# Performance work log

Hardware: AMD Instinct MI355X
Metric: run time of the kernel (lower is better)

Reference implementation:

```python
import jax, jax.numpy as jnp
import numpy as np

B, T, N, D = 64, 10, 64, 4      # batch, time steps, num_vars, input_size
H = 128                          # encoder_hidden
K = 2                            # num_edge_types
EPS = 1e-5                       # BatchNorm eps
_edges = np.ones((N, N)) - np.eye(N)
SEND = jnp.asarray(np.where(_edges)[0])   # [E], E = N*(N-1)
RECV = jnp.asarray(np.where(_edges)[1])   # [E]


def _xavier(key, shape):
    std = (2.0 / (shape[0] + shape[1])) ** 0.5
    return std * jax.random.normal(key, shape, dtype=jnp.float32)


def _mlp(x, w1, b1, w2, b2, g, beta):
    # RefNRIMLP: Linear -> ELU -> (dropout p=0) -> Linear -> ELU -> BatchNorm1d
    h = jax.nn.elu(x @ w1 + b1)
    h = jax.nn.elu(h @ w2 + b2)
    flat = h.reshape(-1, h.shape[-1])  # BN over flattened (batch*objects) axis
    mu = flat.mean(0)
    var = flat.var(0)
    flat = (flat - mu) * jax.lax.rsqrt(var + EPS) * g + beta
    return flat.reshape(h.shape)


def setup_inputs() -> dict:
    key = jax.random.key(0)
    ks = jax.random.split(key, 10)
    inp = {"inputs": jax.random.normal(ks[0], (B, T, N, D), dtype=jnp.float32)}
    fan_ins = {"mlp1": T * D, "mlp2": 2 * H, "mlp3": H, "mlp4": 3 * H}
    for i, (name, nin) in enumerate(fan_ins.items()):
        k1, k2 = jax.random.split(ks[i + 1])
        inp[name + "_w1"] = _xavier(k1, (nin, H))
        inp[name + "_b1"] = jnp.full((H,), 0.1, dtype=jnp.float32)
        inp[name + "_w2"] = _xavier(k2, (H, H))
        inp[name + "_b2"] = jnp.full((H,), 0.1, dtype=jnp.float32)
        inp[name + "_g"] = jnp.ones((H,), dtype=jnp.float32)
        inp[name + "_beta"] = jnp.zeros((H,), dtype=jnp.float32)
    inp["fc_w"] = _xavier(ks[9], (H, K))
    inp["fc_b"] = jnp.full((K,), 0.1, dtype=jnp.float32)
    return inp


def reference(inputs, mlp1_w1, mlp1_b1, mlp1_w2, mlp1_b2, mlp1_g, mlp1_beta,
              mlp2_w1, mlp2_b1, mlp2_w2, mlp2_b2, mlp2_g, mlp2_beta,
              mlp3_w1, mlp3_b1, mlp3_w2, mlp3_b2, mlp3_g, mlp3_beta,
              mlp4_w1, mlp4_b1, mlp4_w2, mlp4_b2, mlp4_g, mlp4_beta,
              fc_w, fc_b):
    # [B,T,N,D] -> [B,N,T*D]
    x = jnp.transpose(inputs, (0, 2, 1, 3)).reshape(B, N, T * D)
    x = _mlp(x, mlp1_w1, mlp1_b1, mlp1_w2, mlp1_b2, mlp1_g, mlp1_beta)
    # node2edge: gather send/recv node embeddings, concat -> [B,E,2H]
    x = jnp.concatenate([x[:, SEND], x[:, RECV]], axis=-1)
    x = _mlp(x, mlp2_w1, mlp2_b1, mlp2_w2, mlp2_b2, mlp2_g, mlp2_beta)
    x_skip = x
    # edge2node: one-hot(recv).T matmul == segment_sum over recv index, then /(N-1)
    agg = jax.ops.segment_sum(jnp.swapaxes(x, 0, 1), RECV, num_segments=N)  # [N,B,H]
    x = jnp.swapaxes(agg, 0, 1) / (N - 1)  # [B,N,H]
    x = _mlp(x, mlp3_w1, mlp3_b1, mlp3_w2, mlp3_b2, mlp3_g, mlp3_beta)
    x = jnp.concatenate([x[:, SEND], x[:, RECV]], axis=-1)  # [B,E,2H]
    x = jnp.concatenate([x, x_skip], axis=-1)  # [B,E,3H]
    x = _mlp(x, mlp4_w1, mlp4_b1, mlp4_w2, mlp4_b2, mlp4_g, mlp4_beta)
    return x @ fc_w + fc_b  # logits [B, E, K]
```

## Files before the change

kernel.cpp:

```cpp
#include <hip/hip_runtime.h>

#define BN_EPS 1e-5f

using h8 = __attribute__((ext_vector_type(8))) _Float16;
using h4v = __attribute__((ext_vector_type(4))) _Float16;
using f4v = __attribute__((ext_vector_type(4))) float;

#define OFF_COEF 0
#define OFF_CVEC 1024
#define OFF_H1 4096
#define OFF_P2 528384
#define OFF_Q2 1052672
#define OFF_H3 1576960
#define OFF_P4 2101248
#define OFF_Q4 2625536
#define OFF_W2P 3149824
#define OFF_W4P 3158016
#define OFF_WCP 3166208
#define OFF_H4B 3174400
#define WS_BYTES 78757888ull

__device__ __forceinline__ float elu_f(float x) {
    return x > 0.f ? x : __expf(x) - 1.f;
}


__device__ __forceinline__ void gemm32_globalW(const float* As, int lda,
                                               const float* __restrict__ Wg, int K,
                                               float acc[2][8], int tx, int ty) {
    const float4* Wg4 = (const float4*)Wg;
#pragma unroll 4
    for (int k = 0; k < K; ++k) {
        float a0 = As[ty * lda + k];
        float a1 = As[(ty + 16) * lda + k];
        float4 wa = Wg4[k * 32 + tx];
        float4 wb = Wg4[k * 32 + 16 + tx];
        const float wv[8] = {wa.x, wa.y, wa.z, wa.w, wb.x, wb.y, wb.z, wb.w};
#pragma unroll
        for (int u = 0; u < 8; ++u) {
            acc[0][u] = fmaf(a0, wv[u], acc[0][u]);
            acc[1][u] = fmaf(a1, wv[u], acc[1][u]);
        }
    }
}

__device__ __forceinline__ void bias_elu32(const float acc[2][8],
                                           const float* __restrict__ bias,
                                           float vals[2][8], int tx) {
    int ca = 4 * tx, cb = 64 + 4 * tx;
    float bv[8] = {bias[ca], bias[ca + 1], bias[ca + 2], bias[ca + 3],
                   bias[cb], bias[cb + 1], bias[cb + 2], bias[cb + 3]};
#pragma unroll
    for (int j = 0; j < 2; ++j)
#pragma unroll
        for (int u = 0; u < 8; ++u)
            vals[j][u] = elu_f(acc[j][u] + bv[u]);
}

__device__ __forceinline__ void store_tile32(float* __restrict__ out, int row0,
                                             const float vals[2][8], int tx, int ty) {
#pragma unroll
    for (int j = 0; j < 2; ++j) {
        int r = row0 + ty + 16 * j;
        *(float4*)(out + r * 128 + 4 * tx) =
            make_float4(vals[j][0], vals[j][1], vals[j][2], vals[j][3]);
        *(float4*)(out + r * 128 + 64 + 4 * tx) =
            make_float4(vals[j][4], vals[j][5], vals[j][6], vals[j][7]);
    }
}

__device__ __forceinline__ void stats_tail32(const float vals[2][8], float* red,
                                             float* __restrict__ st, int tid, int tx, int ty) {
    float ls[8], lq[8];
#pragma unroll
    for (int u = 0; u < 8; ++u) {
        ls[u] = vals[0][u] + vals[1][u];
        lq[u] = vals[0][u] * vals[0][u] + vals[1][u] * vals[1][u];
    }
    __syncthreads();
    int ca = 4 * tx, cb = 64 + 4 * tx;
#pragma unroll
    for (int u = 0; u < 4; ++u) {
        red[ty * 128 + ca + u] = ls[u];
        red[2048 + ty * 128 + ca + u] = lq[u];
        red[ty * 128 + cb + u] = ls[u + 4];
        red[2048 + ty * 128 + cb + u] = lq[u + 4];
    }
    __syncthreads();
    if (tid < 128) {
        float s = 0.f, q = 0.f;
#pragma unroll
        for (int t = 0; t < 16; ++t) {
            s += red[t * 128 + tid];
            q += red[2048 + t * 128 + tid];
        }
        atomicAdd(st + tid, s);
        atomicAdd(st + 128 + tid, q);
    }
}


__device__ __forceinline__ void gemm2_gw(const _Float16* A0, const _Float16* A1,
                                         const _Float16* __restrict__ wp,
                                         f4v acc0[4][2], f4v acc1[4][2], int lane, int w) {
#pragma unroll
    for (int kc = 0; kc < 4; ++kc) {
        h8 bf0 = *(const h8*)&wp[(((w * 2 + 0) * 4 + kc) * 64 + lane) * 8];
        h8 bf1 = *(const h8*)&wp[(((w * 2 + 1) * 4 + kc) * 64 + lane) * 8];
        h8 af0[4], af1[4];
#pragma unroll
        for (int rt = 0; rt < 4; ++rt) {
            af0[rt] = *(const h8*)&A0[((rt * 4 + kc) * 64 + lane) * 8];
            af1[rt] = *(const h8*)&A1[((rt * 4 + kc) * 64 + lane) * 8];
        }
#pragma unroll
        for (int rt = 0; rt < 4; ++rt) {
            acc0[rt][0] = __builtin_amdgcn_mfma_f32_16x16x32_f16(af0[rt], bf0, acc0[rt][0], 0, 0, 0);
            acc1[rt][0] = __builtin_amdgcn_mfma_f32_16x16x32_f16(af1[rt], bf0, acc1[rt][0], 0, 0, 0);
        }
#pragma unroll
        for (int rt = 0; rt < 4; ++rt) {
            acc0[rt][1] = __builtin_amdgcn_mfma_f32_16x16x32_f16(af0[rt], bf1, acc0[rt][1], 0, 0, 0);
            acc1[rt][1] = __builtin_amdgcn_mfma_f32_16x16x32_f16(af1[rt], bf1, acc1[rt][1], 0, 0, 0);
        }
    }
}

__device__ __forceinline__ void vals_to_afrag(_Float16* Afr, const float vals[4][2][4],
                                              int lane, int w) {
    int cl = lane & 15, quad = lane >> 4;
#pragma unroll
    for (int ctl = 0; ctl < 2; ++ctl) {
        int col = (w * 2 + ctl) * 16 + cl;
        int kc = col >> 5, o = (col >> 3) & 3, j = col & 7;
#pragma unroll
        for (int rt = 0; rt < 4; ++rt)
#pragma unroll
            for (int i = 0; i < 4; ++i) {
                int m = quad * 4 + i;
                Afr[((rt * 4 + kc) * 64 + o * 16 + m) * 8 + j] = (_Float16)vals[rt][ctl][i];
            }
    }
}

__device__ __forceinline__ void stage_pair(_Float16* Afr, const float4* __restrict__ Pr,
                                           const float4* __restrict__ Qr,
                                           const float4* __restrict__ B1, int lane, int kc) {
    int rt = lane >> 4, m = lane & 15;
#pragma unroll
    for (int o = 0; o < 4; ++o) {
        int c4 = kc * 8 + o * 2;
        float4 p0 = Pr[c4], q0 = Qr[c4], bb0 = B1[c4];
        float4 p1 = Pr[c4 + 1], q1 = Qr[c4 + 1], bb1 = B1[c4 + 1];
        h8 v;
        v[0] = (_Float16)elu_f(p0.x + q0.x + bb0.x);
        v[1] = (_Float16)elu_f(p0.y + q0.y + bb0.y);
        v[2] = (_Float16)elu_f(p0.z + q0.z + bb0.z);
        v[3] = (_Float16)elu_f(p0.w + q0.w + bb0.w);
        v[4] = (_Float16)elu_f(p1.x + q1.x + bb1.x);
        v[5] = (_Float16)elu_f(p1.y + q1.y + bb1.y);
        v[6] = (_Float16)elu_f(p1.z + q1.z + bb1.z);
        v[7] = (_Float16)elu_f(p1.w + q1.w + bb1.w);
        *(h8*)&Afr[((rt * 4 + kc) * 64 + o * 16 + m) * 8] = v;
    }
}


__global__ void k_prep(float* W, const float* __restrict__ w2src,
                       const float* __restrict__ w4src) {
    int blk = blockIdx.x, tid = threadIdx.x;
    if (blk < 193) {
        int i = blk * 256 + tid;
        if (i < 16384) W[OFF_P2 + i] = 0.f;
        else if (i < 32768) W[OFF_P4 + i - 16384] = 0.f;
        else if (i < 49152) W[OFF_Q4 + i - 32768] = 0.f;
        else if (i < 49280) W[OFF_CVEC + i - 49152] = 0.f;
    } else {
        int second = blk >= 201;
        const float* src = second ? w4src : w2src;
        _Float16* wp = (_Float16*)(W + (second ? OFF_W4P : OFF_W2P));
        int flat = (blk - (second ? 201 : 193)) * 256 + tid;
        int g = flat >> 6, L = flat & 63;
        int ct = g >> 2, kc = g & 3;
        int nn = ct * 16 + (L & 15), k0 = kc * 32 + (L >> 4) * 8;
        h8 v;
#pragma unroll
        for (int j = 0; j < 8; ++j) v[j] = (_Float16)src[(k0 + j) * 128 + nn];
        *(h8*)&wp[flat * 8] = v;
    }
}

__global__ void k_finalize(const float* __restrict__ sums, float* __restrict__ coef,
                           float invM, const float* __restrict__ g,
                           const float* __restrict__ beta, float* __restrict__ zbuf) {
    int c = threadIdx.x;
    float s = 0.f, q = 0.f;
#pragma unroll 8
    for (int t = 0; t < 64; ++t) {
        s += sums[t * 256 + c];
        q += sums[t * 256 + 128 + c];
    }
    float mean = s * invM;
    float var = q * invM - mean * mean;
    float a = g[c] * rsqrtf(var + BN_EPS);
    coef[c] = a;
    coef[128 + c] = beta[c] - mean * a;
    if (zbuf)
        for (int i = c; i < 16384; i += 128) zbuf[i] = 0.f;
}

__global__ __launch_bounds__(256) void k_mlp1(const float* __restrict__ x,
                                              const float* __restrict__ w1,
                                              const float* __restrict__ b1,
                                              const float* __restrict__ w2,
                                              const float* __restrict__ b2,
                                              float* __restrict__ h1, float* __restrict__ st) {
    __shared__ float Xs[32 * 44];
    __shared__ float As[32 * 132];
    int tid = threadIdx.x, tx = tid & 15, ty = tid >> 4;
    int r0 = blockIdx.x * 32;
    for (int idx = tid; idx < 32 * 40; idx += 256) {
        int r = idx / 40, k = idx - r * 40;
        int rr = r0 + r, b = rr >> 6, n = rr & 63, t = k >> 2, d = k & 3;
        Xs[r * 44 + k] = x[((b * 10 + t) * 64 + n) * 4 + d];
    }
    __syncthreads();
    float acc[2][8] = {};
    gemm32_globalW(Xs, 44, w1, 40, acc, tx, ty);
    float vals[2][8];
    bias_elu32(acc, b1, vals, tx);
    int ca = 4 * tx, cb = 64 + 4 * tx;
#pragma unroll
    for (int j = 0; j < 2; ++j) {
        int r = ty + 16 * j;
#pragma unroll
        for (int u = 0; u < 4; ++u) {
            As[r * 132 + ca + u] = vals[j][u];
            As[r * 132 + cb + u] = vals[j][u + 4];
        }
    }
    __syncthreads();
    float acc2[2][8] = {};
    gemm32_globalW(As, 132, w2, 128, acc2, tx, ty);
    float vals2[2][8];
    bias_elu32(acc2, b2, vals2, tx);
    store_tile32(h1, r0, vals2, tx, ty);
    stats_tail32(vals2, As, st + (blockIdx.x & 63) * 256, tid, tx, ty);
}

__global__ __launch_bounds__(256) void k_pq(const float* __restrict__ h,
                                            const float* __restrict__ coef,
                                            const float* __restrict__ w,
                                            float* __restrict__ P, float* __restrict__ Q) {
    __shared__ float As[32 * 132];
    int tid = threadIdx.x, tx = tid & 15, ty = tid >> 4;
    int half = blockIdx.x >> 7;
    int r0 = (blockIdx.x & 127) * 32;
    const float* Wg = w + half * 128 * 128;
    float* out = half ? Q : P;
    const float4* h4 = (const float4*)h;
    const float4* av = (const float4*)coef;
    const float4* cv = (const float4*)(coef + 128);
#pragma unroll
    for (int i = 0; i < 4; ++i) {
        int f4 = tid + i * 256;
        int r = f4 >> 5, c4 = f4 & 31;
        float4 hv = h4[(r0 + r) * 32 + c4];
        float4 a = av[c4], c = cv[c4];
        float4 v;
        v.x = a.x * hv.x + c.x;
        v.y = a.y * hv.y + c.y;
        v.z = a.z * hv.z + c.z;
        v.w = a.w * hv.w + c.w;
        *(float4*)(As + r * 132 + c4 * 4) = v;
    }
    __syncthreads();
    float acc[2][8] = {};
    gemm32_globalW(As, 132, Wg, 128, acc, tx, ty);
#pragma unroll
    for (int j = 0; j < 2; ++j) {
        int r = r0 + ty + 16 * j;
        *(float4*)(out + r * 128 + 4 * tx) = make_float4(acc[j][0], acc[j][1], acc[j][2], acc[j][3]);
        *(float4*)(out + r * 128 + 64 + 4 * tx) = make_float4(acc[j][4], acc[j][5], acc[j][6], acc[j][7]);
    }
}

__global__ __launch_bounds__(256, 3) void k_mlp2agg(const float* __restrict__ P2,
                                                    const float* __restrict__ Q2,
                                                    const float* __restrict__ b1,
                                                    const _Float16* __restrict__ w2p,
                                                    const float* __restrict__ b2,
                                                    float* __restrict__ aggraw,
                                                    _Float16* __restrict__ h2,
                                                    float* __restrict__ st) {
    __shared__ _Float16 Afr0[8192];
    __shared__ _Float16 Afr1[8192];
    int tid = threadIdx.x;
    int lane = tid & 63, w = tid >> 6, cl = lane & 15, quad = lane >> 4;
    int b = blockIdx.x >> 5, j2 = blockIdx.x & 31;
    int n0 = 2 * j2, n1 = n0 + 1;
    float* stc = st + (blockIdx.x & 63) * 256;
    {
        int r = lane;
        int s0 = (r < 63) ? (r + (r >= n0 ? 1 : 0)) : n0;
        int s1i = (r < 63) ? (r + (r >= n1 ? 1 : 0)) : n1;
        const float4* B1 = (const float4*)b1;
        stage_pair(Afr0, (const float4*)(P2 + (b * 64 + s0) * 128),
                   (const float4*)(Q2 + (b * 64 + n0) * 128), B1, lane, w);
        stage_pair(Afr1, (const float4*)(P2 + (b * 64 + s1i) * 128),
                   (const float4*)(Q2 + (b * 64 + n1) * 128), B1, lane, w);
    }
    __syncthreads();
    f4v acc0[4][2], acc1[4][2];
#pragma unroll
    for (int rt = 0; rt < 4; ++rt)
#pragma unroll
        for (int c = 0; c < 2; ++c) {
            acc0[rt][c] = (f4v){0.f, 0.f, 0.f, 0.f};
            acc1[rt][c] = (f4v){0.f, 0.f, 0.f, 0.f};
        }
    gemm2_gw(Afr0, Afr1, w2p, acc0, acc1, lane, w);
    float v0[2][4][4], v1[2][4][4];
#pragma unroll
    for (int ctl = 0; ctl < 2; ++ctl) {
        int col = (w * 2 + ctl) * 16 + cl;
        float bias = b2[col];
        float a0 = 0.f, a1 = 0.f, sq = 0.f;
#pragma unroll
        for (int rt = 0; rt < 4; ++rt)
#pragma unroll
            for (int i = 0; i < 4; ++i) {
                int row = rt * 16 + quad * 4 + i;
                float va = elu_f(acc0[rt][ctl][i] + bias);
                float vb = elu_f(acc1[rt][ctl][i] + bias);
                if (row == 63) { va = 0.f; vb = 0.f; }
                v0[ctl][rt][i] = va;
                v1[ctl][rt][i] = vb;
                a0 += va;
                a1 += vb;
                sq += va * va + vb * vb;
            }
        a0 += __shfl_xor(a0, 16);
        a1 += __shfl_xor(a1, 16);
        sq += __shfl_xor(sq, 16);
        a0 += __shfl_xor(a0, 32);
        a1 += __shfl_xor(a1, 32);
        sq += __shfl_xor(sq, 32);
        if (quad == 0) {
            aggraw[(b * 64 + n0) * 128 + col] = a0;
            aggraw[(b * 64 + n1) * 128 + col] = a1;
            atomicAdd(stc + col, a0 + a1);
            atomicAdd(stc + 128 + col, sq);
        }
    }
    __syncthreads();
    unsigned short* T0 = (unsigned short*)Afr0;
    unsigned short* T1 = (unsigned short*)Afr1;
#pragma unroll
    for (int ctl = 0; ctl < 2; ++ctl) {
        int col = (w * 2 + ctl) * 16 + cl;
#pragma unroll
        for (int rt = 0; rt < 4; ++rt)
#pragma unroll
            for (int i = 0; i < 4; ++i) {
                int row = rt * 16 + quad * 4 + i;
                _Float16 ha = (_Float16)v0[ctl][rt][i];
                _Float16 hb = (_Float16)v1[ctl][rt][i];
                T0[row * 128 + col] = *(unsigned short*)&ha;
                T1[row * 128 + col] = *(unsigned short*)&hb;
            }
    }
    __syncthreads();
    {
        int rr = tid >> 2, cq = tid & 3;
        if (rr < 63) {
            int s0 = rr + (rr >= n0 ? 1 : 0);
            int e0 = s0 * 63 + (s0 > n0 ? n0 : n0 - 1);
            int s1i = rr + (rr >= n1 ? 1 : 0);
            int e1 = s1i * 63 + (s1i > n1 ? n1 : n1 - 1);
            unsigned short* d0 = (unsigned short*)h2 + ((size_t)b * 4032 + e0) * 128;
            unsigned short* d1 = (unsigned short*)h2 + ((size_t)b * 4032 + e1) * 128;
#pragma unroll
            for (int i = 0; i < 4; ++i) {
                int off = cq * 32 + i * 8;
                *(uint4*)(d0 + off) = *(uint4*)&T0[rr * 128 + off];
                *(uint4*)(d1 + off) = *(uint4*)&T1[rr * 128 + off];
            }
        }
    }
}

__global__ void k_wcprep(const float* __restrict__ w41, const float* __restrict__ coef2,
                         _Float16* __restrict__ wcp, float* __restrict__ cvec) {
    int k = blockIdx.x, c = threadIdx.x;
    float wv = w41[(256 + k) * 128 + c];
    int g = (c >> 4) * 4 + (k >> 5);
    int L = ((k >> 3) & 3) * 16 + (c & 15);
    int j = k & 7;
    wcp[(g * 64 + L) * 8 + j] = (_Float16)(coef2[k] * wv);
    atomicAdd(&cvec[c], coef2[128 + k] * wv);
}

__global__ __launch_bounds__(256) void k_mlp3(const float* __restrict__ raw,
                                              const float* __restrict__ coef2,
                                              const float* __restrict__ w1,
                                              const float* __restrict__ b1,
                                              const float* __restrict__ w2,
                                              const float* __restrict__ b2,
                                              float* __restrict__ h3, float* __restrict__ st) {
    __shared__ float As[32 * 132];
    int tid = threadIdx.x, tx = tid & 15, ty = tid >> 4;
    int r0 = blockIdx.x * 32;
    const float4* in4 = (const float4*)raw;
    const float4* av = (const float4*)coef2;
    const float4* cv = (const float4*)(coef2 + 128);
    const float inv63 = 1.f / 63.f;
#pragma unroll
    for (int i = 0; i < 4; ++i) {
        int f4 = tid + i * 256;
        int r = f4 >> 5, c4 = f4 & 31;
        float4 hv = in4[(r0 + r) * 32 + c4];
        float4 a = av[c4], c = cv[c4];
        float4 v;
        v.x = a.x * hv.x * inv63 + c.x;
        v.y = a.y * hv.y * inv63 + c.y;
        v.z = a.z * hv.z * inv63 + c.z;
        v.w = a.w * hv.w * inv63 + c.w;
        *(float4*)(As + r * 132 + c4 * 4) = v;
    }
    __syncthreads();
    float acc[2][8] = {};
    gemm32_globalW(As, 132, w1, 128, acc, tx, ty);
    float vals[2][8];
    bias_elu32(acc, b1, vals, tx);
    __syncthreads();
    int ca = 4 * tx, cb = 64 + 4 * tx;
#pragma unroll
    for (int j = 0; j < 2; ++j) {
        int r = ty + 16 * j;
#pragma unroll
        for (int u = 0; u < 4; ++u) {
            As[r * 132 + ca + u] = vals[j][u];
            As[r * 132 + cb + u] = vals[j][u + 4];
        }
    }
    __syncthreads();
    float acc2[2][8] = {};
    gemm32_globalW(As, 132, w2, 128, acc2, tx, ty);
    float vals2[2][8];
    bias_elu32(acc2, b2, vals2, tx);
    store_tile32(h3, r0, vals2, tx, ty);
    stats_tail32(vals2, As, st + (blockIdx.x & 63) * 256, tid, tx, ty);
}

__global__ __launch_bounds__(256, 3) void k_mlp4r2(const _Float16* __restrict__ h2,
                                                   const float* __restrict__ P4,
                                                   const float* __restrict__ Q4,
                                                   const _Float16* __restrict__ wcp,
                                                   const float* __restrict__ cvec,
                                                   const float* __restrict__ b1,
                                                   const _Float16* __restrict__ w4p2,
                                                   const float* __restrict__ b2,
                                                   unsigned short* __restrict__ h4,
                                                   float* __restrict__ st) {
    __shared__ _Float16 Afr0[8192];
    __shared__ _Float16 Afr1[8192];
    int tid = threadIdx.x;
    int lane = tid & 63, w = tid >> 6, cl = lane & 15, quad = lane >> 4;
    unsigned t0 = 2u * blockIdx.x, t1 = t0 + 1u;
    unsigned b0 = t0 / 63, b1i = t1 / 63;
    unsigned e00 = (t0 - b0 * 63) * 64, e01 = (t1 - b1i * 63) * 64;
    int row00 = t0 * 64, row01 = t1 * 64;
    float* stc = st + (blockIdx.x & 63) * 256;
#pragma unroll
    for (int i = 0; i < 4; ++i) {
        int u = tid + i * 256;
        int r = u >> 4, cu = u & 15;
        int dst = (((r >> 4) * 4 + (cu >> 2)) * 64 + (cu & 3) * 16 + (r & 15)) * 8;
        *(h8*)&Afr0[dst] = *(const h8*)&h2[(size_t)(row00 + r) * 128 + cu * 8];
        *(h8*)&Afr1[dst] = *(const h8*)&h2[(size_t)(row01 + r) * 128 + cu * 8];
    }
    __syncthreads();
    f4v acc0[4][2], acc1[4][2];
#pragma unroll
    for (int rt = 0; rt < 4; ++rt)
#pragma unroll
        for (int c = 0; c < 2; ++c) {
            acc0[rt][c] = (f4v){0.f, 0.f, 0.f, 0.f};
            acc1[rt][c] = (f4v){0.f, 0.f, 0.f, 0.f};
        }
    gemm2_gw(Afr0, Afr1, wcp, acc0, acc1, lane, w);
    float v0[4][2][4], v1[4][2][4];
    {
        int col0 = w * 32 + cl, col1 = col0 + 16;
        float base0 = b1[col0] + cvec[col0];
        float base1 = b1[col1] + cvec[col1];
        unsigned sA0 = e00 / 63, sA1 = e01 / 63;
        unsigned baseE0 = sA0 * 63, baseE1 = sA1 * 63;
        unsigned eB0 = baseE0 + 63, eB1 = baseE1 + 63;
        unsigned sB0 = sA0 < 63u ? sA0 + 1u : sA0;
        unsigned sB1 = sA1 < 63u ? sA1 + 1u : sA1;
        const float* PA0 = P4 + (b0 * 64 + sA0) * 128;
        const float* PB0 = P4 + (b0 * 64 + sB0) * 128;
        const float* PA1 = P4 + (b1i * 64 + sA1) * 128;
        const float* PB1 = P4 + (b1i * 64 + sB1) * 128;
        float pA0c0 = PA0[col0], pA0c1 = PA0[col1];
        float pB0c0 = PB0[col0], pB0c1 = PB0[col1];
        float pA1c0 = PA1[col0], pA1c1 = PA1[col1];
        float pB1c0 = PB1[col0], pB1c1 = PB1[col1];
        const float* Qb0 = Q4 + (size_t)b0 * 8192;
        const float* Qb1 = Q4 + (size_t)b1i * 8192;
#pragma unroll
        for (int rt = 0; rt < 4; ++rt)
#pragma unroll
            for (int i = 0; i < 4; ++i) {
                int rr = rt * 16 + quad * 4 + i;
                {
                    unsigned e = e00 + rr;
                    bool hi = e >= eB0;
                    unsigned s = hi ? sB0 : sA0;
                    unsigned jj = e - (hi ? eB0 : baseE0);
                    unsigned rv = jj + (jj >= s ? 1u : 0u);
                    const float* Qr = Qb0 + rv * 128;
                    float p0 = hi ? pB0c0 : pA0c0, p1 = hi ? pB0c1 : pA0c1;
                    v0[rt][0][i] = elu_f(acc0[rt][0][i] + p0 + Qr[col0] + base0);
                    v0[rt][1][i] = elu_f(acc0[rt][1][i] + p1 + Qr[col1] + base1);
                }
                {
                    unsigned e = e01 + rr;
                    bool hi = e >= eB1;
                    unsigned s = hi ? sB1 : sA1;
                    unsigned jj = e - (hi ? eB1 : baseE1);
                    unsigned rv = jj + (jj >= s ? 1u : 0u);
                    const float* Qr = Qb1 + rv * 128;
                    float p0 = hi ? pB1c0 : pA1c0, p1 = hi ? pB1c1 : pA1c1;
                    v1[rt][0][i] = elu_f(acc1[rt][0][i] + p0 + Qr[col0] + base0);
                    v1[rt][1][i] = elu_f(acc1[rt][1][i] + p1 + Qr[col1] + base1);
                }
            }
    }
    __syncthreads();
    vals_to_afrag(Afr0, v0, lane, w);
    vals_to_afrag(Afr1, v1, lane, w);
    __syncthreads();
#pragma unroll
    for (int rt = 0; rt < 4; ++rt)
#pragma unroll
        for (int c = 0; c < 2; ++c) {
            acc0[rt][c] = (f4v){0.f, 0.f, 0.f, 0.f};
            acc1[rt][c] = (f4v){0.f, 0.f, 0.f, 0.f};
        }
    gemm2_gw(Afr0, Afr1, w4p2, acc0, acc1, lane, w);
#pragma unroll
    for (int ctl = 0; ctl < 2; ++ctl) {
        int col = (w * 2 + ctl) * 16 + cl;
        float bias = b2[col];
        float s1 = 0.f, s2 = 0.f;
#pragma unroll
        for (int rt = 0; rt < 4; ++rt)
#pragma unroll
            for (int i = 0; i < 4; ++i) {
                float va = elu_f(acc0[rt][ctl][i] + bias);
                float vb = elu_f(acc1[rt][ctl][i] + bias);
                v0[rt][ctl][i] = va;
                v1[rt][ctl][i] = vb;
                s1 += va + vb;
                s2 += va * va + vb * vb;
            }
        s1 += __shfl_xor(s1, 16);
        s2 += __shfl_xor(s2, 16);
        s1 += __shfl_xor(s1, 32);
        s2 += __shfl_xor(s2, 32);
        if (quad == 0) {
            atomicAdd(stc + col, s1);
            atomicAdd(stc + 128 + col, s2);
        }
    }
    __syncthreads();
    unsigned short* T0 = (unsigned short*)Afr0;
    unsigned short* T1 = (unsigned short*)Afr1;
#pragma unroll
    for (int ctl = 0; ctl < 2; ++ctl) {
        int col = (w * 2 + ctl) * 16 + cl;
#pragma unroll
        for (int rt = 0; rt < 4; ++rt)
#pragma unroll
            for (int i = 0; i < 4; ++i) {
                int rr = rt * 16 + quad * 4 + i;
                _Float16 ha = (_Float16)v0[rt][ctl][i];
                _Float16 hb = (_Float16)v1[rt][ctl][i];
                T0[rr * 128 + col] = *(unsigned short*)&ha;
                T1[rr * 128 + col] = *(unsigned short*)&hb;
            }
    }
    __syncthreads();
    {
        int rr = tid >> 2, cq = tid & 3;
#pragma unroll
        for (int i = 0; i < 4; ++i) {
            int off = rr * 128 + cq * 32 + i * 8;
            *(uint4*)(h4 + (size_t)row00 * 128 + off) = *(uint4*)&T0[off];
            *(uint4*)(h4 + (size_t)row01 * 128 + off) = *(uint4*)&T1[off];
        }
    }
}

__global__ __launch_bounds__(256) void k_out(const unsigned short* __restrict__ h4,
                                             const float* __restrict__ coef4,
                                             const float* __restrict__ fcw,
                                             const float* __restrict__ fcb,
                                             float* __restrict__ out) {
    int tid = threadIdx.x;
    int lane = tid & 31, rsub = tid >> 5;
    int row = blockIdx.x * 8 + rsub;
    h4v hv = ((const h4v*)(h4 + (size_t)row * 128))[lane];
    float x0 = (float)hv[0], x1 = (float)hv[1], x2 = (float)hv[2], x3 = (float)hv[3];
    float4 a = ((const float4*)coef4)[lane];
    float4 c = ((const float4*)(coef4 + 128))[lane];
    x0 = a.x * x0 + c.x;
    x1 = a.y * x1 + c.y;
    x2 = a.z * x2 + c.z;
    x3 = a.w * x3 + c.w;
    const float4* W = (const float4*)(fcw + lane * 8);
    float4 w01 = W[0], w23 = W[1];
    float s0 = x0 * w01.x + x1 * w01.z + x2 * w23.x + x3 * w23.z;
    float s1 = x0 * w01.y + x1 * w01.w + x2 * w23.y + x3 * w23.w;
#pragma unroll
    for (int off = 16; off > 0; off >>= 1) {
        s0 += __shfl_down(s0, off, 32);
        s1 += __shfl_down(s1, off, 32);
    }
    if (lane == 0) {
        out[row * 2] = s0 + fcb[0];
        out[row * 2 + 1] = s1 + fcb[1];
    }
}


extern "C" void kernel_launch(void* const* d_in, const int* in_sizes, int n_in,
                              void* d_out, int out_size, void* d_ws, size_t ws_size,
                              hipStream_t stream) {
    const float* x = (const float*)d_in[0];
    const float* m1_w1 = (const float*)d_in[1];
    const float* m1_b1 = (const float*)d_in[2];
    const float* m1_w2 = (const float*)d_in[3];
    const float* m1_b2 = (const float*)d_in[4];
    const float* m1_g = (const float*)d_in[5];
    const float* m1_be = (const float*)d_in[6];
    const float* m2_w1 = (const float*)d_in[7];
    const float* m2_b1 = (const float*)d_in[8];
    const float* m2_w2 = (const float*)d_in[9];
    const float* m2_b2 = (const float*)d_in[10];
    const float* m2_g = (const float*)d_in[11];
    const float* m2_be = (const float*)d_in[12];
    const float* m3_w1 = (const float*)d_in[13];
    const float* m3_b1 = (const float*)d_in[14];
    const float* m3_w2 = (const float*)d_in[15];
    const float* m3_b2 = (const float*)d_in[16];
    const float* m3_g = (const float*)d_in[17];
    const float* m3_be = (const float*)d_in[18];
    const float* m4_w1 = (const float*)d_in[19];
    const float* m4_b1 = (const float*)d_in[20];
    const float* m4_w2 = (const float*)d_in[21];
    const float* m4_b2 = (const float*)d_in[22];
    const float* m4_g = (const float*)d_in[23];
    const float* m4_be = (const float*)d_in[24];
    const float* fc_w = (const float*)d_in[25];
    const float* fc_b = (const float*)d_in[26];
    float* out = (float*)d_out;

    float* W = (float*)d_ws;
    float* coef1 = W + OFF_COEF;
    float* coef2 = W + OFF_COEF + 256;
    float* coef3 = W + OFF_COEF + 512;
    float* coef4 = W + OFF_COEF + 768;
    float* cvec = W + OFF_CVEC;
    float* h1 = W + OFF_H1;
    float* aggraw = h1;
    float* sums4 = h1;
    float* P2 = W + OFF_P2;
    float* sums1 = P2;
    float* Q2 = W + OFF_Q2;
    float* h3 = W + OFF_H3;
    float* P4 = W + OFF_P4;
    float* sums2 = P4;
    float* Q4 = W + OFF_Q4;
    float* sums3 = Q4;
    _Float16* w2p2 = (_Float16*)(W + OFF_W2P);
    _Float16* w4p2 = (_Float16*)(W + OFF_W4P);
    _Float16* wcp = (_Float16*)(W + OFF_WCP);
    _Float16* h2f = (_Float16*)(W + OFF_H4B);
    unsigned short* h4b = (unsigned short*)(W + OFF_H4B);

    if (ws_size < WS_BYTES) return;

    k_prep<<<209, 256, 0, stream>>>(W, m2_w2, m4_w2);
    k_mlp1<<<128, 256, 0, stream>>>(x, m1_w1, m1_b1, m1_w2, m1_b2, h1, sums1);
    k_finalize<<<1, 128, 0, stream>>>(sums1, coef1, 1.f / 4096.f, m1_g, m1_be, nullptr);
    k_pq<<<256, 256, 0, stream>>>(h1, coef1, m2_w1, P2, Q2);
    k_mlp2agg<<<2048, 256, 0, stream>>>(P2, Q2, m2_b1, w2p2, m2_b2, aggraw, h2f, sums2);
    k_finalize<<<1, 128, 0, stream>>>(sums2, coef2, 1.f / 258048.f, m2_g, m2_be, nullptr);
    k_wcprep<<<128, 128, 0, stream>>>(m4_w1, coef2, wcp, cvec);
    k_mlp3<<<128, 256, 0, stream>>>(aggraw, coef2, m3_w1, m3_b1, m3_w2, m3_b2, h3, sums3);
    k_finalize<<<1, 128, 0, stream>>>(sums3, coef3, 1.f / 4096.f, m3_g, m3_be, sums4);
    k_pq<<<256, 256, 0, stream>>>(h3, coef3, m4_w1, P4, Q4);
    k_mlp4r2<<<2016, 256, 0, stream>>>(h2f, P4, Q4, wcp, cvec, m4_b1, w4p2, m4_b2,
                                       h4b, sums4);
    k_finalize<<<1, 128, 0, stream>>>(sums4, coef4, 1.f / 258048.f, m4_g, m4_be, nullptr);
    k_out<<<32256, 256, 0, stream>>>(h4b, coef4, fc_w, fc_b, out);
}
```

Baseline: 346.4 us.

## Fold BatchNorm finalize and prep kernels into neighboring kernels to cut launches

Removes the separate prep and four single-block finalize kernels. Weight packing and zeroing move into extra blocks of the first MLP kernel, and each BN coefficient computation is recomputed per block inside the consuming kernel (pq, wc prep, output). Small-MLP stats now go to per-block slots instead of atomics, and the output kernel processes 256 rows per block with far fewer blocks. This cuts launch and serialization gaps but adds redundant per-block reductions over the stat slots, and workspace aliasing is reshuffled.

```diff
diff --git a/kernel.cpp b/kernel.cpp
--- a/kernel.cpp
+++ b/kernel.cpp
@@ -69,8 +69,9 @@
     }
 }
 
-__device__ __forceinline__ void stats_tail32(const float vals[2][8], float* red,
-                                             float* __restrict__ st, int tid, int tx, int ty) {
+__device__ __forceinline__ void stats_tail32_store(const float vals[2][8], float* red,
+                                                   float* __restrict__ slot, int tid,
+                                                   int tx, int ty) {
     float ls[8], lq[8];
 #pragma unroll
     for (int u = 0; u < 8; ++u) {
@@ -94,8 +95,8 @@
             s += red[t * 128 + tid];
             q += red[2048 + t * 128 + tid];
         }
-        atomicAdd(st + tid, s);
-        atomicAdd(st + 128 + tid, q);
+        slot[tid] = s;
+        slot[128 + tid] = q;
     }
 }
 
@@ -166,59 +167,45 @@
 }
 
 
-__global__ void k_prep(float* W, const float* __restrict__ w2src,
-                       const float* __restrict__ w4src) {
-    int blk = blockIdx.x, tid = threadIdx.x;
-    if (blk < 193) {
-        int i = blk * 256 + tid;
-        if (i < 16384) W[OFF_P2 + i] = 0.f;
-        else if (i < 32768) W[OFF_P4 + i - 16384] = 0.f;
-        else if (i < 49152) W[OFF_Q4 + i - 32768] = 0.f;
-        else if (i < 49280) W[OFF_CVEC + i - 49152] = 0.f;
-    } else {
-        int second = blk >= 201;
-        const float* src = second ? w4src : w2src;
-        _Float16* wp = (_Float16*)(W + (second ? OFF_W4P : OFF_W2P));
-        int flat = (blk - (second ? 201 : 193)) * 256 + tid;
-        int g = flat >> 6, L = flat & 63;
-        int ct = g >> 2, kc = g & 3;
-        int nn = ct * 16 + (L & 15), k0 = kc * 32 + (L >> 4) * 8;
-        h8 v;
-#pragma unroll
-        for (int j = 0; j < 8; ++j) v[j] = (_Float16)src[(k0 + j) * 128 + nn];
-        *(h8*)&wp[flat * 8] = v;
-    }
-}
-
-__global__ void k_finalize(const float* __restrict__ sums, float* __restrict__ coef,
-                           float invM, const float* __restrict__ g,
-                           const float* __restrict__ beta, float* __restrict__ zbuf) {
-    int c = threadIdx.x;
-    float s = 0.f, q = 0.f;
-#pragma unroll 8
-    for (int t = 0; t < 64; ++t) {
-        s += sums[t * 256 + c];
-        q += sums[t * 256 + 128 + c];
-    }
-    float mean = s * invM;
-    float var = q * invM - mean * mean;
-    float a = g[c] * rsqrtf(var + BN_EPS);
-    coef[c] = a;
-    coef[128 + c] = beta[c] - mean * a;
-    if (zbuf)
-        for (int i = c; i < 16384; i += 128) zbuf[i] = 0.f;
-}
-
-__global__ __launch_bounds__(256) void k_mlp1(const float* __restrict__ x,
-                                              const float* __restrict__ w1,
-                                              const float* __restrict__ b1,
-                                              const float* __restrict__ w2,
-                                              const float* __restrict__ b2,
-                                              float* __restrict__ h1, float* __restrict__ st) {
+__global__ __launch_bounds__(256) void k_mlp1p(const float* __restrict__ x,
+                                               const float* __restrict__ w1,
+                                               const float* __restrict__ b1,
+                                               const float* __restrict__ w2,
+                                               const float* __restrict__ b2,
+                                               float* __restrict__ h1,
+                                               float* __restrict__ slots,
+                                               float* __restrict__ sums2,
+                                               float* __restrict__ cvec,
+                                               const float* __restrict__ w2src,
+                                               _Float16* __restrict__ w2p,
+                                               const float* __restrict__ w4src,
+                                               _Float16* __restrict__ w4p) {
     __shared__ float Xs[32 * 44];
     __shared__ float As[32 * 132];
-    int tid = threadIdx.x, tx = tid & 15, ty = tid >> 4;
-    int r0 = blockIdx.x * 32;
+    int tid = threadIdx.x;
+    int blk = blockIdx.x;
+    if (blk >= 128) {
+        if (blk < 193) {
+            int i = (blk - 128) * 256 + tid;
+            if (i < 16384) sums2[i] = 0.f;
+            else if (i < 16512) cvec[i - 16384] = 0.f;
+        } else {
+            int second = blk >= 201;
+            const float* src = second ? w4src : w2src;
+            _Float16* wp = second ? w4p : w2p;
+            int flat = (blk - (second ? 201 : 193)) * 256 + tid;
+            int g = flat >> 6, L = flat & 63;
+            int ct = g >> 2, kc = g & 3;
+            int nn = ct * 16 + (L & 15), k0 = kc * 32 + (L >> 4) * 8;
+            h8 v;
+#pragma unroll
+            for (int j = 0; j < 8; ++j) v[j] = (_Float16)src[(k0 + j) * 128 + nn];
+            *(h8*)&wp[flat * 8] = v;
+        }
+        return;
+    }
+    int tx = tid & 15, ty = tid >> 4;
+    int r0 = blk * 32;
     for (int idx = tid; idx < 32 * 40; idx += 256) {
         int r = idx / 40, k = idx - r * 40;
         int rr = r0 + r, b = rr >> 6, n = rr & 63, t = k >> 2, d = k & 3;
@@ -245,33 +232,51 @@
     float vals2[2][8];
     bias_elu32(acc2, b2, vals2, tx);
     store_tile32(h1, r0, vals2, tx, ty);
-    stats_tail32(vals2, As, st + (blockIdx.x & 63) * 256, tid, tx, ty);
-}
-
-__global__ __launch_bounds__(256) void k_pq(const float* __restrict__ h,
-                                            const float* __restrict__ coef,
-                                            const float* __restrict__ w,
-                                            float* __restrict__ P, float* __restrict__ Q) {
+    stats_tail32_store(vals2, As, slots + blk * 256, tid, tx, ty);
+}
+
+__global__ __launch_bounds__(256) void k_pqf(const float* __restrict__ h,
+                                             const float* __restrict__ slots,
+                                             const float* __restrict__ g,
+                                             const float* __restrict__ beta,
+                                             const float* __restrict__ w,
+                                             float* __restrict__ P, float* __restrict__ Q,
+                                             float* __restrict__ zero4) {
+    __shared__ float Cf[256];
     __shared__ float As[32 * 132];
     int tid = threadIdx.x, tx = tid & 15, ty = tid >> 4;
     int half = blockIdx.x >> 7;
     int r0 = (blockIdx.x & 127) * 32;
+    if (zero4 && tid < 64) zero4[blockIdx.x * 64 + tid] = 0.f;
+    if (tid < 128) {
+        int c = tid;
+        float s = 0.f, q = 0.f;
+#pragma unroll 8
+        for (int t = 0; t < 128; ++t) {
+            s += slots[t * 256 + c];
+            q += slots[t * 256 + 128 + c];
+        }
+        float mean = s * (1.f / 4096.f);
+        float var = q * (1.f / 4096.f) - mean * mean;
+        float a = g[c] * rsqrtf(var + BN_EPS);
+        Cf[c] = a;
+        Cf[128 + c] = beta[c] - mean * a;
+    }
+    __syncthreads();
     const float* Wg = w + half * 128 * 128;
     float* out = half ? Q : P;
-    const float4* h4 = (const float4*)h;
-    const float4* av = (const float4*)coef;
-    const float4* cv = (const float4*)(coef + 128);
+    const float4* h4p = (const float4*)h;
 #pragma unroll
     for (int i = 0; i < 4; ++i) {
         int f4 = tid + i * 256;
         int r = f4 >> 5, c4 = f4 & 31;
-        float4 hv = h4[(r0 + r) * 32 + c4];
-        float4 a = av[c4], c = cv[c4];
+        float4 hv = h4p[(r0 + r) * 32 + c4];
+        int cb = c4 * 4;
         float4 v;
-        v.x = a.x * hv.x + c.x;
-        v.y = a.y * hv.y + c.y;
-        v.z = a.z * hv.z + c.z;
-        v.w = a.w * hv.w + c.w;
+        v.x = Cf[cb] * hv.x + Cf[128 + cb];
+        v.y = Cf[cb + 1] * hv.y + Cf[128 + cb + 1];
+        v.z = Cf[cb + 2] * hv.z + Cf[128 + cb + 2];
+        v.w = Cf[cb + 3] * hv.w + Cf[128 + cb + 3];
         *(float4*)(As + r * 132 + c4 * 4) = v;
     }
     __syncthreads();
@@ -390,15 +395,41 @@
     }
 }
 
-__global__ void k_wcprep(const float* __restrict__ w41, const float* __restrict__ coef2,
-                         _Float16* __restrict__ wcp, float* __restrict__ cvec) {
+__global__ __launch_bounds__(128) void k_wcfin(const float* __restrict__ sums2,
+                                               const float* __restrict__ g2,
+                                               const float* __restrict__ be2,
+                                               const float* __restrict__ w41,
+                                               _Float16* __restrict__ wcp,
+                                               float* __restrict__ cvec,
+                                               float* __restrict__ coef2) {
+    __shared__ float red[128];
+    __shared__ float pr[2];
     int k = blockIdx.x, c = threadIdx.x;
+    red[c] = (c < 64) ? sums2[c * 256 + k] : sums2[(c - 64) * 256 + 128 + k];
+    __syncthreads();
+    if (c == 0) {
+        float s = 0.f, q = 0.f;
+#pragma unroll 8
+        for (int t = 0; t < 64; ++t) {
+            s += red[t];
+            q += red[64 + t];
+        }
+        float mean = s * (1.f / 258048.f);
+        float var = q * (1.f / 258048.f) - mean * mean;
+        float a = g2[k] * rsqrtf(var + BN_EPS);
+        pr[0] = a;
+        pr[1] = be2[k] - mean * a;
+        coef2[k] = a;
+        coef2[128 + k] = pr[1];
+    }
+    __syncthreads();
+    float a2k = pr[0], sh2k = pr[1];
     float wv = w41[(256 + k) * 128 + c];
     int g = (c >> 4) * 4 + (k >> 5);
     int L = ((k >> 3) & 3) * 16 + (c & 15);
     int j = k & 7;
-    wcp[(g * 64 + L) * 8 + j] = (_Float16)(coef2[k] * wv);
-    atomicAdd(&cvec[c], coef2[128 + k] * wv);
+    wcp[(g * 64 + L) * 8 + j] = (_Float16)(a2k * wv);
+    atomicAdd(&cvec[c], sh2k * wv);
 }
 
 __global__ __launch_bounds__(256) void k_mlp3(const float* __restrict__ raw,
@@ -407,7 +438,8 @@
                                               const float* __restrict__ b1,
                                               const float* __restrict__ w2,
                                               const float* __restrict__ b2,
-                                              float* __restrict__ h3, float* __restrict__ st) {
+                                              float* __restrict__ h3,
+                                              float* __restrict__ slots) {
     __shared__ float As[32 * 132];
     int tid = threadIdx.x, tx = tid & 15, ty = tid >> 4;
     int r0 = blockIdx.x * 32;
@@ -450,7 +482,7 @@
     float vals2[2][8];
     bias_elu32(acc2, b2, vals2, tx);
     store_tile32(h3, r0, vals2, tx, ty);
-    stats_tail32(vals2, As, st + (blockIdx.x & 63) * 256, tid, tx, ty);
+    stats_tail32_store(vals2, As, slots + blockIdx.x * 256, tid, tx, ty);
 }
 
 __global__ __launch_bounds__(256, 3) void k_mlp4r2(const _Float16* __restrict__ h2,
@@ -605,34 +637,57 @@
     }
 }
 
-__global__ __launch_bounds__(256) void k_out(const unsigned short* __restrict__ h4,
-                                             const float* __restrict__ coef4,
-                                             const float* __restrict__ fcw,
-                                             const float* __restrict__ fcb,
-                                             float* __restrict__ out) {
+__global__ __launch_bounds__(256) void k_outf(const unsigned short* __restrict__ h4,
+                                              const float* __restrict__ sums4,
+                                              const float* __restrict__ g4,
+                                              const float* __restrict__ be4,
+                                              const float* __restrict__ fcw,
+                                              const float* __restrict__ fcb,
+                                              float* __restrict__ out) {
+    __shared__ float Cf[256];
     int tid = threadIdx.x;
+    if (tid < 128) {
+        int c = tid;
+        float s = 0.f, q = 0.f;
+#pragma unroll 8
+        for (int t = 0; t < 64; ++t) {
+            s += sums4[t * 256 + c];
+            q += sums4[t * 256 + 128 + c];
+        }
+        float mean = s * (1.f / 258048.f);
+        float var = q * (1.f / 258048.f) - mean * mean;
+        float a = g4[c] * rsqrtf(var + BN_EPS);
+        Cf[c] = a;
+        Cf[128 + c] = be4[c] - mean * a;
+    }
+    __syncthreads();
     int lane = tid & 31, rsub = tid >> 5;
-    int row = blockIdx.x * 8 + rsub;
-    h4v hv = ((const h4v*)(h4 + (size_t)row * 128))[lane];
-    float x0 = (float)hv[0], x1 = (float)hv[1], x2 = (float)hv[2], x3 = (float)hv[3];
-    float4 a = ((const float4*)coef4)[lane];
-    float4 c = ((const float4*)(coef4 + 128))[lane];
-    x0 = a.x * x0 + c.x;
-    x1 = a.y * x1 + c.y;
-    x2 = a.z * x2 + c.z;
-    x3 = a.w * x3 + c.w;
-    const float4* W = (const float4*)(fcw + lane * 8);
-    float4 w01 = W[0], w23 = W[1];
-    float s0 = x0 * w01.x + x1 * w01.z + x2 * w23.x + x3 * w23.z;
-    float s1 = x0 * w01.y + x1 * w01.w + x2 * w23.y + x3 * w23.w;
-#pragma unroll
-    for (int off = 16; off > 0; off >>= 1) {
-        s0 += __shfl_down(s0, off, 32);
-        s1 += __shfl_down(s1, off, 32);
-    }
-    if (lane == 0) {
-        out[row * 2] = s0 + fcb[0];
-        out[row * 2 + 1] = s1 + fcb[1];
+    const float4* Wp = (const float4*)(fcw + lane * 8);
+    float4 w01 = Wp[0], w23 = Wp[1];
+    float fb0 = fcb[0], fb1 = fcb[1];
+    float a0 = Cf[lane * 4], a1 = Cf[lane * 4 + 1], a2 = Cf[lane * 4 + 2], a3 = Cf[lane * 4 + 3];
+    float c0 = Cf[128 + lane * 4], c1 = Cf[128 + lane * 4 + 1];
+    float c2 = Cf[128 + lane * 4 + 2], c3 = Cf[128 + lane * 4 + 3];
+    size_t base = (size_t)blockIdx.x * 256;
+#pragma unroll 4
+    for (int it = 0; it < 32; ++it) {
+        size_t row = base + it * 8 + rsub;
+        h4v hv = ((const h4v*)(h4 + row * 128))[lane];
+        float x0 = a0 * (float)hv[0] + c0;
+        float x1 = a1 * (float)hv[1] + c1;
+        float x2 = a2 * (float)hv[2] + c2;
+        float x3 = a3 * (float)hv[3] + c3;
+        float s0 = x0 * w01.x + x1 * w01.z + x2 * w23.x + x3 * w23.z;
+        float s1 = x0 * w01.y + x1 * w01.w + x2 * w23.y + x3 * w23.w;
+#pragma unroll
+        for (int off = 16; off > 0; off >>= 1) {
+            s0 += __shfl_down(s0, off, 32);
+            s1 += __shfl_down(s1, off, 32);
+        }
+        if (lane == 0) {
+            out[row * 2] = s0 + fb0;
+            out[row * 2 + 1] = s1 + fb1;
+        }
     }
 }
 
@@ -670,22 +725,19 @@
     float* out = (float*)d_out;
 
     float* W = (float*)d_ws;
-    float* coef1 = W + OFF_COEF;
-    float* coef2 = W + OFF_COEF + 256;
-    float* coef3 = W + OFF_COEF + 512;
-    float* coef4 = W + OFF_COEF + 768;
+    float* coef2 = W + OFF_COEF;
     float* cvec = W + OFF_CVEC;
     float* h1 = W + OFF_H1;
     float* aggraw = h1;
     float* sums4 = h1;
     float* P2 = W + OFF_P2;
-    float* sums1 = P2;
+    float* sums3 = P2;
     float* Q2 = W + OFF_Q2;
     float* h3 = W + OFF_H3;
+    float* sums1 = h3;
     float* P4 = W + OFF_P4;
     float* sums2 = P4;
     float* Q4 = W + OFF_Q4;
-    float* sums3 = Q4;
     _Float16* w2p2 = (_Float16*)(W + OFF_W2P);
     _Float16* w4p2 = (_Float16*)(W + OFF_W4P);
     _Float16* wcp = (_Float16*)(W + OFF_WCP);
@@ -694,18 +746,14 @@
 
     if (ws_size < WS_BYTES) return;
 
-    k_prep<<<209, 256, 0, stream>>>(W, m2_w2, m4_w2);
-    k_mlp1<<<128, 256, 0, stream>>>(x, m1_w1, m1_b1, m1_w2, m1_b2, h1, sums1);
-    k_finalize<<<1, 128, 0, stream>>>(sums1, coef1, 1.f / 4096.f, m1_g, m1_be, nullptr);
-    k_pq<<<256, 256, 0, stream>>>(h1, coef1, m2_w1, P2, Q2);
+    k_mlp1p<<<209, 256, 0, stream>>>(x, m1_w1, m1_b1, m1_w2, m1_b2, h1, sums1,
+                                     sums2, cvec, m2_w2, w2p2, m4_w2, w4p2);
+    k_pqf<<<256, 256, 0, stream>>>(h1, sums1, m1_g, m1_be, m2_w1, P2, Q2, nullptr);
     k_mlp2agg<<<2048, 256, 0, stream>>>(P2, Q2, m2_b1, w2p2, m2_b2, aggraw, h2f, sums2);
-    k_finalize<<<1, 128, 0, stream>>>(sums2, coef2, 1.f / 258048.f, m2_g, m2_be, nullptr);
-    k_wcprep<<<128, 128, 0, stream>>>(m4_w1, coef2, wcp, cvec);
+    k_wcfin<<<128, 128, 0, stream>>>(sums2, m2_g, m2_be, m4_w1, wcp, cvec, coef2);
     k_mlp3<<<128, 256, 0, stream>>>(aggraw, coef2, m3_w1, m3_b1, m3_w2, m3_b2, h3, sums3);
-    k_finalize<<<1, 128, 0, stream>>>(sums3, coef3, 1.f / 4096.f, m3_g, m3_be, sums4);
-    k_pq<<<256, 256, 0, stream>>>(h3, coef3, m4_w1, P4, Q4);
+    k_pqf<<<256, 256, 0, stream>>>(h3, sums3, m3_g, m3_be, m4_w1, P4, Q4, sums4);
     k_mlp4r2<<<2016, 256, 0, stream>>>(h2f, P4, Q4, wcp, cvec, m4_b1, w4p2, m4_b2,
                                        h4b, sums4);
-    k_finalize<<<1, 128, 0, stream>>>(sums4, coef4, 1.f / 258048.f, m4_g, m4_be, nullptr);
-    k_out<<<32256, 256, 0, stream>>>(h4b, coef4, fc_w, fc_b, out);
-}
+    k_outf<<<1008, 256, 0, stream>>>(h4b, sums4, m4_g, m4_be, fc_w, fc_b, out);
+}
```

Measured after the change: 338.3 us (median of 2 runs). 2.4% less time.
